# Performance work log

Measured on AMD Instinct MI355X. Metric: run time of the kernel, lower is better.

## Reference

```python
import jax, jax.numpy as jnp
import numpy as np

B, S, H = 2, 2048, 2048
NH, HD = 16, 128


def _rope_tables(seq_len, dim, base=10000.0):
    inv_freq = 1.0 / (base ** (np.arange(0, dim, 2, dtype=np.float32) / dim))
    t = np.arange(seq_len, dtype=np.float32)
    freqs = np.outer(t, inv_freq)                      # [S, dim/2]
    emb = np.concatenate([freqs, freqs], axis=-1)      # [S, dim] (HF convention)
    return jnp.asarray(np.cos(emb)), jnp.asarray(np.sin(emb))


def setup_inputs() -> dict:
    key = jax.random.key(0)
    k1, k2, k3, k4, k5 = jax.random.split(key, 5)
    hidden_states = jax.random.normal(k1, (B, S, H), dtype=jnp.float32)
    # additive causal mask, broadcast over heads: (B, 1, S, S)
    causal = jnp.tril(jnp.ones((S, S), dtype=bool))
    attention_mask = jnp.where(causal, 0.0, -1e9).astype(jnp.float32)
    attention_mask = jnp.broadcast_to(attention_mask[None, None], (B, 1, S, S))
    rope_cos, rope_sin = _rope_tables(S, HD)
    scale = 1.0 / np.sqrt(H)
    Wq = jax.random.normal(k2, (H, H), dtype=jnp.float32) * scale
    Wk = jax.random.normal(k3, (H, H), dtype=jnp.float32) * scale
    Wv = jax.random.normal(k4, (H, H), dtype=jnp.float32) * scale
    Wo = jax.random.normal(k5, (H, H), dtype=jnp.float32) * scale
    return dict(hidden_states=hidden_states, attention_mask=attention_mask,
                rope_cos=rope_cos, rope_sin=rope_sin, Wq=Wq, Wk=Wk, Wv=Wv, Wo=Wo)


def _rotate_half(x):
    half = x.shape[-1] // 2
    return jnp.concatenate([-x[..., half:], x[..., :half]], axis=-1)


def reference(hidden_states, attention_mask, rope_cos, rope_sin, Wq, Wk, Wv, Wo):
    bsz, q_len, _ = hidden_states.shape
    scaling = HD ** -0.5
    # projections (torch Linear: y = x @ W.T)
    q = (hidden_states @ Wq.T).reshape(bsz, q_len, NH, HD).transpose(0, 2, 1, 3)
    k = (hidden_states @ Wk.T).reshape(bsz, q_len, NH, HD).transpose(0, 2, 1, 3)
    v = (hidden_states @ Wv.T).reshape(bsz, q_len, NH, HD).transpose(0, 2, 1, 3)
    # RoPE (rotate_half convention)
    cos = rope_cos[None, None]  # [1,1,S,HD]
    sin = rope_sin[None, None]
    q = q * cos + _rotate_half(q) * sin
    k = k * cos + _rotate_half(k) * sin
    # attention
    scores = jnp.einsum('bhqd,bhkd->bhqk', q, k) * scaling + attention_mask
    attn = jax.nn.softmax(scores.astype(jnp.float32), axis=-1).astype(q.dtype)
    out = jnp.einsum('bhqk,bhkd->bhqd', attn, v)
    out = out.transpose(0, 2, 1, 3).reshape(bsz, q_len, NH * HD)
    return out @ Wo.T
```

## Files before the change

### kernel.cpp

```cpp
#include <hip/hip_runtime.h>
#include <hip/hip_bf16.h>

typedef __bf16 bf16;
typedef __attribute__((ext_vector_type(8))) __bf16 bf16x8;
typedef __attribute__((ext_vector_type(4))) __bf16 bf16x4;
typedef __attribute__((ext_vector_type(4))) float f32x4;

#define BB 2
#define SS 2048
#define HH 2048
#define NH 16
#define HD 128

#define GLOAD_LDS16(g, l)                                                  \
    __builtin_amdgcn_global_load_lds(                                      \
        (const __attribute__((address_space(1))) void*)(g),                \
        (__attribute__((address_space(3))) void*)(l), 16, 0, 0)

__global__ __launch_bounds__(256) void cast_all(const float* __restrict__ hs,
                                                const float* __restrict__ Wq,
                                                const float* __restrict__ Wk,
                                                const float* __restrict__ Wv,
                                                const float* __restrict__ Wo,
                                                bf16* __restrict__ Xb,
                                                bf16* __restrict__ Wqkv,
                                                bf16* __restrict__ Wob) {
    const int XE4 = (BB * SS * HH) / 4;
    const int WE4 = (HH * HH) / 4;
    int i = blockIdx.x * 256 + threadIdx.x;
    const float* src;
    bf16* dst;
    int off;
    if (i < XE4) { src = hs; dst = Xb; off = i; }
    else if (i < XE4 + WE4) { src = Wq; dst = Wqkv; off = i - XE4; }
    else if (i < XE4 + 2 * WE4) { src = Wk; dst = Wqkv + (size_t)HH * HH; off = i - XE4 - WE4; }
    else if (i < XE4 + 3 * WE4) { src = Wv; dst = Wqkv + 2 * (size_t)HH * HH; off = i - XE4 - 2 * WE4; }
    else { src = Wo; dst = Wob; off = i - XE4 - 3 * WE4; }
    f32x4 v = *reinterpret_cast<const f32x4*>(src + (size_t)off * 4);
    bf16x4 o;
    o[0] = (bf16)v[0]; o[1] = (bf16)v[1]; o[2] = (bf16)v[2]; o[3] = (bf16)v[3];
    *reinterpret_cast<bf16x4*>(dst + (size_t)off * 4) = o;
}

__global__ __launch_bounds__(512, 2) void gemm256_qkv(const bf16* __restrict__ A,
                                                      const bf16* __restrict__ B,
                                                      bf16* __restrict__ Cb,
                                                      int M, int N, int K) {
    __shared__ bf16 LA[2][256 * 64];
    __shared__ bf16 LB[2][256 * 64];
    const int tid = threadIdx.x, lane = tid & 63, wave = tid >> 6;
    const int l15 = lane & 15, lhi = lane >> 4;
    const int wr = wave >> 2, wc = wave & 3;
    const int NBY = M >> 8;
    const int cpx = gridDim.x >> 3;
    const int wg = (blockIdx.x & 7) * cpx + (blockIdx.x >> 3);
    const int m0 = (wg % NBY) * 256, n0 = (wg / NBY) * 256;
    const int NK = K >> 6;
    const int xorR = (l15 & 7) << 4;

    auto stageA = [&](int buf, int t, int h) {
        const int k0 = t << 6;
#pragma unroll
        for (int j = 0; j < 2; ++j) {
            int Xw = ((j * 128 + h * 64) << 7) + (wave << 10);
            int X = Xw + lane * 16;
            int T = X ^ (((X >> 7) & 7) << 4);
            GLOAD_LDS16(&A[(size_t)(m0 + (T >> 7)) * K + k0 + ((T & 127) >> 1)],
                        (char*)LA[buf] + Xw);
        }
    };
    auto stageB = [&](int buf, int t, int h) {
        const int k0 = t << 6;
#pragma unroll
        for (int j = 0; j < 2; ++j) {
            int base_row = h * 32 + (2 * j + (wave >> 2)) * 64;
            int Xw = (base_row << 7) + ((wave & 3) << 10);
            int X = Xw + lane * 16;
            int T = X ^ (((X >> 7) & 7) << 4);
            GLOAD_LDS16(&B[(size_t)(n0 + (T >> 7)) * K + k0 + ((T & 127) >> 1)],
                        (char*)LB[buf] + Xw);
        }
    };

    f32x4 acc[8][4] = {};

    stageA(0, 0, 0); stageB(0, 0, 0); stageB(0, 0, 1); stageA(0, 0, 1);
    stageA(1, 1, 0); stageB(1, 1, 1);
    asm volatile("s_waitcnt vmcnt(4)" ::: "memory");
    __builtin_amdgcn_s_barrier();

    bf16x8 af[4][2], bv0[2][2], bv1[2][2];

#pragma unroll 1
    for (int t = 0; t < NK; ++t) {
        const int buf = t & 1;
        char* lA = (char*)LA[buf];
        char* lB = (char*)LB[buf];

#pragma unroll
        for (int f = 0; f < 4; ++f)
#pragma unroll
            for (int ks = 0; ks < 2; ++ks) {
                int T = ((wr * 128 + f * 16 + l15) << 7) + ks * 64 + lhi * 16;
                af[f][ks] = *reinterpret_cast<const bf16x8*>(lA + (T ^ xorR));
            }
#pragma unroll
        for (int g = 0; g < 2; ++g)
#pragma unroll
            for (int ks = 0; ks < 2; ++ks) {
                int T = ((wc * 64 + g * 16 + l15) << 7) + ks * 64 + lhi * 16;
                bv0[g][ks] = *reinterpret_cast<const bf16x8*>(lB + (T ^ xorR));
            }
        if (t + 1 < NK) stageB(buf ^ 1, t + 1, 0);
        __builtin_amdgcn_s_barrier();
        __builtin_amdgcn_s_setprio(1);
#pragma unroll
        for (int f = 0; f < 4; ++f)
#pragma unroll
            for (int g = 0; g < 2; ++g)
#pragma unroll
                for (int ks = 0; ks < 2; ++ks)
                    acc[f][g] = __builtin_amdgcn_mfma_f32_16x16x32_bf16(af[f][ks], bv0[g][ks], acc[f][g], 0, 0, 0);
        __builtin_amdgcn_s_setprio(0);
        __builtin_amdgcn_s_barrier();

#pragma unroll
        for (int g = 0; g < 2; ++g)
#pragma unroll
            for (int ks = 0; ks < 2; ++ks) {
                int T = ((wc * 64 + 32 + g * 16 + l15) << 7) + ks * 64 + lhi * 16;
                bv1[g][ks] = *reinterpret_cast<const bf16x8*>(lB + (T ^ xorR));
            }
        if (t + 1 < NK) stageA(buf ^ 1, t + 1, 1);
        __builtin_amdgcn_s_barrier();
        __builtin_amdgcn_s_setprio(1);
#pragma unroll
        for (int f = 0; f < 4; ++f)
#pragma unroll
            for (int g = 0; g < 2; ++g)
#pragma unroll
                for (int ks = 0; ks < 2; ++ks)
                    acc[f][2 + g] = __builtin_amdgcn_mfma_f32_16x16x32_bf16(af[f][ks], bv1[g][ks], acc[f][2 + g], 0, 0, 0);
        __builtin_amdgcn_s_setprio(0);
        __builtin_amdgcn_s_barrier();

#pragma unroll
        for (int f = 0; f < 4; ++f)
#pragma unroll
            for (int ks = 0; ks < 2; ++ks) {
                int T = ((wr * 128 + 64 + f * 16 + l15) << 7) + ks * 64 + lhi * 16;
                af[f][ks] = *reinterpret_cast<const bf16x8*>(lA + (T ^ xorR));
            }
        if (t + 2 < NK) stageA(buf, t + 2, 0);
        __builtin_amdgcn_s_barrier();
        __builtin_amdgcn_s_setprio(1);
#pragma unroll
        for (int f = 0; f < 4; ++f)
#pragma unroll
            for (int g = 0; g < 2; ++g)
#pragma unroll
                for (int ks = 0; ks < 2; ++ks)
                    acc[4 + f][2 + g] = __builtin_amdgcn_mfma_f32_16x16x32_bf16(af[f][ks], bv1[g][ks], acc[4 + f][2 + g], 0, 0, 0);
        __builtin_amdgcn_s_setprio(0);
        __builtin_amdgcn_s_barrier();

        if (t + 2 < NK) stageB(buf, t + 2, 1);
        __builtin_amdgcn_s_barrier();
        __builtin_amdgcn_s_setprio(1);
#pragma unroll
        for (int f = 0; f < 4; ++f)
#pragma unroll
            for (int g = 0; g < 2; ++g)
#pragma unroll
                for (int ks = 0; ks < 2; ++ks)
                    acc[4 + f][g] = __builtin_amdgcn_mfma_f32_16x16x32_bf16(af[f][ks], bv0[g][ks], acc[4 + f][g], 0, 0, 0);
        __builtin_amdgcn_s_setprio(0);
        if (t + 2 == NK) {
            asm volatile("s_waitcnt vmcnt(0)" ::: "memory");
        } else if (t + 1 < NK) {
            asm volatile("s_waitcnt vmcnt(4)" ::: "memory");
        }
        __builtin_amdgcn_s_barrier();
    }

#pragma unroll
    for (int mf = 0; mf < 8; ++mf)
#pragma unroll
        for (int nf = 0; nf < 4; ++nf)
#pragma unroll
            for (int r = 0; r < 4; ++r) {
                int gm = m0 + wr * 128 + mf * 16 + lhi * 4 + r;
                int gn = n0 + wc * 64 + nf * 16 + l15;
                int proj = gn >> 11, n2 = gn & 2047;
                int b = gm >> 11, s = gm & (SS - 1);
                int h = n2 >> 7, d = n2 & (HD - 1);
                Cb[((size_t)proj << 23) + ((((size_t)(b * NH + h)) * SS + s) << 7) + d] =
                    (bf16)acc[mf][nf][r];
            }
}

__global__ __launch_bounds__(256) void gemm_bt(const bf16* __restrict__ A,
                                               const bf16* __restrict__ B,
                                               float* __restrict__ Cf,
                                               int M, int N, int K) {
    __shared__ bf16 As[128 * 64];
    __shared__ bf16 Bs[128 * 64];
    const int tid = threadIdx.x;
    const int lane = tid & 63, wave = tid >> 6;
    const int l15 = lane & 15, lhi = lane >> 4;
    const int m0 = blockIdx.y * 128, n0 = blockIdx.x * 128;
    const int wm = (wave >> 1) * 64, wn = (wave & 1) * 64;
    const int lrow = lane >> 3;
    const int lcol = (lane & 7) * 8;

    f32x4 acc[4][4] = {};

    for (int k0 = 0; k0 < K; k0 += 64) {
#pragma unroll
        for (int j = 0; j < 4; ++j) {
            const int c = wave * 4 + j;
            const int row = c * 8 + lrow;
            GLOAD_LDS16(&A[(size_t)(m0 + row) * K + k0 + lcol], &As[c * 512]);
            GLOAD_LDS16(&B[(size_t)(n0 + row) * K + k0 + lcol], &Bs[c * 512]);
        }
        __syncthreads();
#pragma unroll
        for (int ks = 0; ks < 2; ++ks) {
            bf16x8 af[4], bfr[4];
#pragma unroll
            for (int i = 0; i < 4; ++i)
                af[i] = *reinterpret_cast<const bf16x8*>(&As[(wm + i * 16 + l15) * 64 + ks * 32 + 8 * lhi]);
#pragma unroll
            for (int j = 0; j < 4; ++j)
                bfr[j] = *reinterpret_cast<const bf16x8*>(&Bs[(wn + j * 16 + l15) * 64 + ks * 32 + 8 * lhi]);
#pragma unroll
            for (int i = 0; i < 4; ++i)
#pragma unroll
                for (int j = 0; j < 4; ++j)
                    acc[i][j] = __builtin_amdgcn_mfma_f32_16x16x32_bf16(af[i], bfr[j], acc[i][j], 0, 0, 0);
        }
        __syncthreads();
    }

#pragma unroll
    for (int i = 0; i < 4; ++i)
#pragma unroll
        for (int j = 0; j < 4; ++j)
#pragma unroll
            for (int r = 0; r < 4; ++r) {
                int gm = m0 + wm + i * 16 + lhi * 4 + r;
                int gn = n0 + wn + j * 16 + l15;
                Cf[(size_t)gm * N + gn] = acc[i][j][r];
            }
}

__global__ __launch_bounds__(256) void rope_tv(bf16* __restrict__ Qh,
                                               bf16* __restrict__ Kh,
                                               const float* __restrict__ cosT,
                                               const float* __restrict__ sinT,
                                               const bf16* __restrict__ Vh,
                                               bf16* __restrict__ Vt) {
    __shared__ bf16 T[64 * 64];
    const int tid = threadIdx.x;
    if (blockIdx.x < 2048) {
        int idx = blockIdx.x * 256 + tid;
        int g = idx & 7;
        int s = (idx >> 3) & (SS - 1);
        int head = idx >> 14;
        int d0 = g * 8;
        size_t base = ((size_t)head * SS + s) * HD;
        f32x4 ca = *reinterpret_cast<const f32x4*>(&cosT[s * HD + d0]);
        f32x4 cb = *reinterpret_cast<const f32x4*>(&cosT[s * HD + d0 + 4]);
        f32x4 sa = *reinterpret_cast<const f32x4*>(&sinT[s * HD + d0]);
        f32x4 sb = *reinterpret_cast<const f32x4*>(&sinT[s * HD + d0 + 4]);
        bf16x8 ql = *reinterpret_cast<const bf16x8*>(&Qh[base + d0]);
        bf16x8 qh = *reinterpret_cast<const bf16x8*>(&Qh[base + 64 + d0]);
        bf16x8 kl = *reinterpret_cast<const bf16x8*>(&Kh[base + d0]);
        bf16x8 kh = *reinterpret_cast<const bf16x8*>(&Kh[base + 64 + d0]);
        bf16x8 qlo, qhi, klo, khi;
#pragma unroll
        for (int j = 0; j < 8; ++j) {
            float c = (j < 4) ? ca[j] : cb[j - 4];
            float sn = (j < 4) ? sa[j] : sb[j - 4];
            float q0 = (float)ql[j], q1 = (float)qh[j];
            float k0 = (float)kl[j], k1 = (float)kh[j];
            qlo[j] = (bf16)(q0 * c - q1 * sn);
            qhi[j] = (bf16)(q1 * c + q0 * sn);
            klo[j] = (bf16)(k0 * c - k1 * sn);
            khi[j] = (bf16)(k1 * c + k0 * sn);
        }
        *reinterpret_cast<bf16x8*>(&Qh[base + d0]) = qlo;
        *reinterpret_cast<bf16x8*>(&Qh[base + 64 + d0]) = qhi;
        *reinterpret_cast<bf16x8*>(&Kh[base + d0]) = klo;
        *reinterpret_cast<bf16x8*>(&Kh[base + 64 + d0]) = khi;
    } else {
        const int b2 = blockIdx.x - 2048;
        const int s0 = (b2 & 31) * 64;
        const int d0 = ((b2 >> 5) & 1) * 64;
        const int head = b2 >> 6;
        const bf16* src = Vh + ((size_t)head * SS) * HD;
        bf16* dst = Vt + ((size_t)head * HD) * SS;

#pragma unroll
        for (int i = 0; i < 2; ++i) {
            int id = tid + i * 256;
            int r = id >> 3, c16 = id & 7;
            bf16x8 v = *reinterpret_cast<const bf16x8*>(&src[(size_t)(s0 + r) * HD + d0 + c16 * 8]);
            int sw = c16 ^ ((r ^ (r >> 3)) & 7);
            *reinterpret_cast<bf16x8*>((char*)T + r * 128 + sw * 16) = v;
        }
        __syncthreads();
#pragma unroll
        for (int i = 0; i < 2; ++i) {
            int id = tid + i * 256;
            int dr = id >> 3, sc8 = (id & 7) * 8;
            bf16x8 o;
#pragma unroll
            for (int j = 0; j < 8; ++j) {
                int r = sc8 + j;
                int sw = (dr >> 3) ^ ((r ^ (r >> 3)) & 7);
                o[j] = *reinterpret_cast<const bf16*>((char*)T + r * 128 + sw * 16 + (dr & 7) * 2);
            }
            *reinterpret_cast<bf16x8*>(&dst[(size_t)(d0 + dr) * SS + s0 + sc8]) = o;
        }
    }
}

__global__ __launch_bounds__(256) void attn_kernel(const bf16* __restrict__ Q,
                                                   const bf16* __restrict__ K,
                                                   const bf16* __restrict__ Vt,
                                                   bf16* __restrict__ Ob) {
    __shared__ bf16 Ks[2][64 * 128];
    __shared__ bf16 Vs[2][128 * 64];
    __shared__ bf16 Ps[4][16][72];

    const int tid = threadIdx.x, lane = tid & 63, wave = tid >> 6;
    const int l15 = lane & 15, lhi = lane >> 4;
    const int bid = blockIdx.x;
    const int orig = (bid & 7) * 64 + (bid >> 3);
    const int head = orig >> 4;
    const int pi = orig & 15;
    const int b = head >> 4, h = head & (NH - 1);
    const size_t hb = (size_t)head * SS * HD;
    const bf16* Vth = Vt + (size_t)head * HD * SS;
    const float cexp = 0.08838834764831845f * 1.4426950408889634f;
    const float THR = 62.0f;

#pragma unroll 1
    for (int part = 0; part < 2; ++part) {
        const int t = part ? (31 - pi) : pi;
        const int q0 = t * 64;
        const int qw = q0 + wave * 16;
        const int nkv = t + 1;

        bf16x8 qf[4];
#pragma unroll
        for (int ks = 0; ks < 4; ++ks)
            qf[ks] = *reinterpret_cast<const bf16x8*>(
                &Q[hb + (size_t)(qw + l15) * HD + ks * 32 + 8 * lhi]);

        f32x4 oacc[8] = {};
        float Mr[4], Lp[4];
#pragma unroll
        for (int r = 0; r < 4; ++r) { Mr[r] = -INFINITY; Lp[r] = 0.f; }

        bf16x8 kr[4], vr[4];
#pragma unroll
        for (int i = 0; i < 4; ++i) {
            int id = tid + i * 256;
            kr[i] = *reinterpret_cast<const bf16x8*>(&K[hb + (size_t)(id >> 4) * HD + (id & 15) * 8]);
            vr[i] = *reinterpret_cast<const bf16x8*>(&Vth[(size_t)(id >> 3) * SS + (id & 7) * 8]);
        }
#pragma unroll
        for (int i = 0; i < 4; ++i) {
            int id = tid + i * 256;
            int krow = id >> 4, kc = id & 15;
            *reinterpret_cast<bf16x8*>((char*)Ks[0] + ((krow * 256 + kc * 16) ^ ((krow & 7) << 4))) = kr[i];
            int vrow = id >> 3, vc = id & 7;
            *reinterpret_cast<bf16x8*>((char*)Vs[0] + ((vrow * 128 + vc * 16) ^ ((vrow & 7) << 4))) = vr[i];
        }
        __syncthreads();

        for (int it = 0; it < nkv; ++it) {
            const int cur = it & 1;
            const bool pre = (it + 1 < nkv);
            if (pre) {
                const int kv0 = (it + 1) * 64;
#pragma unroll
                for (int i = 0; i < 4; ++i) {
                    int id = tid + i * 256;
                    kr[i] = *reinterpret_cast<const bf16x8*>(&K[hb + (size_t)(kv0 + (id >> 4)) * HD + (id & 15) * 8]);
                    vr[i] = *reinterpret_cast<const bf16x8*>(&Vth[(size_t)(id >> 3) * SS + kv0 + (id & 7) * 8]);
                }
            }

            f32x4 sf[4] = {};
#pragma unroll
            for (int ks = 0; ks < 4; ++ks) {
#pragma unroll
                for (int ne = 0; ne < 4; ++ne) {
                    int row = ne * 16 + l15;
                    bf16x8 kf = *reinterpret_cast<const bf16x8*>(
                        (const char*)Ks[cur] + ((row * 256 + (ks * 4 + lhi) * 16) ^ ((row & 7) << 4)));
                    sf[ne] = __builtin_amdgcn_mfma_f32_16x16x32_bf16(qf[ks], kf, sf[ne], 0, 0, 0);
                }
            }

            if (it == nkv - 1) {
#pragma unroll
                for (int ne = 0; ne < 4; ++ne)
#pragma unroll
                    for (int r = 0; r < 4; ++r) {
                        int gq = qw + lhi * 4 + r;
                        int gk = it * 64 + ne * 16 + l15;
                        if (gk > gq) sf[ne][r] = -INFINITY;
                    }
            }

            float lm[4];
#pragma unroll
            for (int r = 0; r < 4; ++r)
                lm[r] = fmaxf(fmaxf(sf[0][r], sf[1][r]), fmaxf(sf[2][r], sf[3][r]));
            bool need = (lm[0] > Mr[0] + THR) || (lm[1] > Mr[1] + THR) ||
                        (lm[2] > Mr[2] + THR) || (lm[3] > Mr[3] + THR);
            if (__any(need)) {
                float rmax[4] = {lm[0], lm[1], lm[2], lm[3]};
#pragma unroll
                for (int m = 1; m < 16; m <<= 1)
#pragma unroll
                    for (int r = 0; r < 4; ++r)
                        rmax[r] = fmaxf(rmax[r], __shfl_xor(rmax[r], m));
#pragma unroll
                for (int r = 0; r < 4; ++r) {
                    float nM = fmaxf(Mr[r], rmax[r]);
                    float scf = __builtin_amdgcn_exp2f((Mr[r] - nM) * cexp);
                    Mr[r] = nM;
                    Lp[r] *= scf;
#pragma unroll
                    for (int nf = 0; nf < 8; ++nf) oacc[nf][r] *= scf;
                }
            }
#pragma unroll
            for (int ne = 0; ne < 4; ++ne)
#pragma unroll
                for (int r = 0; r < 4; ++r) {
                    float p = __builtin_amdgcn_exp2f((sf[ne][r] - Mr[r]) * cexp);
                    Lp[r] += p;
                    Ps[wave][lhi * 4 + r][ne * 16 + l15] = (bf16)p;
                }

#pragma unroll
            for (int ks = 0; ks < 2; ++ks) {
                bf16x8 pa = *reinterpret_cast<const bf16x8*>(&Ps[wave][l15][ks * 32 + 8 * lhi]);
#pragma unroll
                for (int nf = 0; nf < 8; ++nf) {
                    int row = nf * 16 + l15;
                    bf16x8 vb = *reinterpret_cast<const bf16x8*>(
                        (const char*)Vs[cur] + ((row * 128 + (ks * 4 + lhi) * 16) ^ ((row & 7) << 4)));
                    oacc[nf] = __builtin_amdgcn_mfma_f32_16x16x32_bf16(pa, vb, oacc[nf], 0, 0, 0);
                }
            }

            if (pre) {
#pragma unroll
                for (int i = 0; i < 4; ++i) {
                    int id = tid + i * 256;
                    int krow = id >> 4, kc = id & 15;
                    *reinterpret_cast<bf16x8*>((char*)Ks[cur ^ 1] + ((krow * 256 + kc * 16) ^ ((krow & 7) << 4))) = kr[i];
                    int vrow = id >> 3, vc = id & 7;
                    *reinterpret_cast<bf16x8*>((char*)Vs[cur ^ 1] + ((vrow * 128 + vc * 16) ^ ((vrow & 7) << 4))) = vr[i];
                }
            }
            __syncthreads();
        }

#pragma unroll
        for (int m = 1; m < 16; m <<= 1)
#pragma unroll
            for (int r = 0; r < 4; ++r)
                Lp[r] += __shfl_xor(Lp[r], m);
        float inv[4];
#pragma unroll
        for (int r = 0; r < 4; ++r) inv[r] = 1.f / Lp[r];
#pragma unroll
        for (int nf = 0; nf < 8; ++nf)
#pragma unroll
            for (int r = 0; r < 4; ++r) {
                int s = qw + lhi * 4 + r;
                int d = nf * 16 + l15;
                Ob[((size_t)(b * SS + s)) * HH + h * HD + d] = (bf16)(oacc[nf][r] * inv[r]);
            }
    }
}

extern "C" void kernel_launch(void* const* d_in, const int* in_sizes, int n_in,
                              void* d_out, int out_size, void* d_ws, size_t ws_size,
                              hipStream_t stream) {
    const float* hs   = (const float*)d_in[0];
    const float* cosT = (const float*)d_in[2];
    const float* sinT = (const float*)d_in[3];
    const float* Wq   = (const float*)d_in[4];
    const float* Wk   = (const float*)d_in[5];
    const float* Wv   = (const float*)d_in[6];
    const float* Wo   = (const float*)d_in[7];
    float* out = (float*)d_out;

    char* w = (char*)d_ws;
    auto alloc = [&](size_t bytes) {
        char* p = w;
        w += (bytes + 255) & ~(size_t)255;
        return p;
    };
    const size_t XE = (size_t)BB * SS * HH;
    const size_t WE = (size_t)HH * HH;
    bf16* Xb   = (bf16*)alloc(XE * 2);
    bf16* Wqkv = (bf16*)alloc(3 * WE * 2);
    bf16* Wob  = (bf16*)alloc(WE * 2);
    bf16* QKV  = (bf16*)alloc(3 * XE * 2);
    bf16* Vtg  = (bf16*)alloc(XE * 2);
    bf16* Ob   = (bf16*)alloc(XE * 2);

    const int M = BB * SS;
    bf16* Qh = QKV;
    bf16* Kh = QKV + XE;
    bf16* Vh = QKV + 2 * XE;

    {
        int total4 = (int)((XE + 4 * WE) / 4);
        cast_all<<<(total4 + 255) / 256, 256, 0, stream>>>(hs, Wq, Wk, Wv, Wo, Xb, Wqkv, Wob);
    }

    gemm256_qkv<<<dim3((M / 256) * (3 * HH / 256)), 512, 0, stream>>>(Xb, Wqkv, QKV, M, 3 * HH, HH);

    rope_tv<<<4096, 256, 0, stream>>>(Qh, Kh, cosT, sinT, Vh, Vtg);

    attn_kernel<<<512, 256, 0, stream>>>(Qh, Kh, Vtg, Ob);

    dim3 ogrid(HH / 128, M / 128);
    gemm_bt<<<ogrid, 256, 0, stream>>>(Ob, Wob, out, M, HH, HH);
}
```

Before: 298.4 us.

## Use 128-row query tiles with 8 waves and direct global-to-LDS KV staging

Measured after the change: 273.8 us. 1.09x faster.

```diff
diff --git a/kernel.cpp b/kernel.cpp
--- a/kernel.cpp
+++ b/kernel.cpp
@@ -326,32 +326,51 @@
     }
 }
 
-__global__ __launch_bounds__(256) void attn_kernel(const bf16* __restrict__ Q,
+__global__ __launch_bounds__(512) void attn_kernel(const bf16* __restrict__ Q,
                                                    const bf16* __restrict__ K,
                                                    const bf16* __restrict__ Vt,
                                                    bf16* __restrict__ Ob) {
     __shared__ bf16 Ks[2][64 * 128];
     __shared__ bf16 Vs[2][128 * 64];
-    __shared__ bf16 Ps[4][16][72];
+    __shared__ bf16 Ps[8][16 * 72];
 
     const int tid = threadIdx.x, lane = tid & 63, wave = tid >> 6;
     const int l15 = lane & 15, lhi = lane >> 4;
     const int bid = blockIdx.x;
-    const int orig = (bid & 7) * 64 + (bid >> 3);
-    const int head = orig >> 4;
-    const int pi = orig & 15;
+    const int orig = (bid & 7) * 32 + (bid >> 3);
+    const int head = orig >> 3;
+    const int pi = orig & 7;
     const int b = head >> 4, h = head & (NH - 1);
     const size_t hb = (size_t)head * SS * HD;
     const bf16* Vth = Vt + (size_t)head * HD * SS;
     const float cexp = 0.08838834764831845f * 1.4426950408889634f;
     const float THR = 62.0f;
 
+    auto stageKV = [&](int buf, int kv0) {
+#pragma unroll
+        for (int j = 0; j < 2; ++j) {
+            int Xw = (j * 8 + wave) << 10;
+            int X = Xw + lane * 16;
+            int T = X ^ (((X >> 8) & 7) << 4);
+            GLOAD_LDS16(&K[hb + (size_t)(kv0 + (T >> 8)) * HD + ((T & 255) >> 1)],
+                        (char*)Ks[buf] + Xw);
+        }
+#pragma unroll
+        for (int j = 0; j < 2; ++j) {
+            int Xw = (j * 8 + wave) << 10;
+            int X = Xw + lane * 16;
+            int T = X ^ (((X >> 7) & 7) << 4);
+            GLOAD_LDS16(&Vth[(size_t)(T >> 7) * SS + kv0 + ((T & 127) >> 1)],
+                        (char*)Vs[buf] + Xw);
+        }
+    };
+
 #pragma unroll 1
     for (int part = 0; part < 2; ++part) {
-        const int t = part ? (31 - pi) : pi;
-        const int q0 = t * 64;
+        const int t = part ? (15 - pi) : pi;
+        const int q0 = t * 128;
         const int qw = q0 + wave * 16;
-        const int nkv = t + 1;
+        const int nkv = 2 * t + 2;
 
         bf16x8 qf[4];
 #pragma unroll
@@ -364,35 +383,13 @@
 #pragma unroll
         for (int r = 0; r < 4; ++r) { Mr[r] = -INFINITY; Lp[r] = 0.f; }
 
-        bf16x8 kr[4], vr[4];
-#pragma unroll
-        for (int i = 0; i < 4; ++i) {
-            int id = tid + i * 256;
-            kr[i] = *reinterpret_cast<const bf16x8*>(&K[hb + (size_t)(id >> 4) * HD + (id & 15) * 8]);
-            vr[i] = *reinterpret_cast<const bf16x8*>(&Vth[(size_t)(id >> 3) * SS + (id & 7) * 8]);
-        }
-#pragma unroll
-        for (int i = 0; i < 4; ++i) {
-            int id = tid + i * 256;
-            int krow = id >> 4, kc = id & 15;
-            *reinterpret_cast<bf16x8*>((char*)Ks[0] + ((krow * 256 + kc * 16) ^ ((krow & 7) << 4))) = kr[i];
-            int vrow = id >> 3, vc = id & 7;
-            *reinterpret_cast<bf16x8*>((char*)Vs[0] + ((vrow * 128 + vc * 16) ^ ((vrow & 7) << 4))) = vr[i];
-        }
-        __syncthreads();
+        stageKV(0, 0);
+        asm volatile("s_waitcnt vmcnt(0)" ::: "memory");
+        __builtin_amdgcn_s_barrier();
 
         for (int it = 0; it < nkv; ++it) {
             const int cur = it & 1;
-            const bool pre = (it + 1 < nkv);
-            if (pre) {
-                const int kv0 = (it + 1) * 64;
-#pragma unroll
-                for (int i = 0; i < 4; ++i) {
-                    int id = tid + i * 256;
-                    kr[i] = *reinterpret_cast<const bf16x8*>(&K[hb + (size_t)(kv0 + (id >> 4)) * HD + (id & 15) * 8]);
-                    vr[i] = *reinterpret_cast<const bf16x8*>(&Vth[(size_t)(id >> 3) * SS + kv0 + (id & 7) * 8]);
-                }
-            }
+            if (it + 1 < nkv) stageKV(cur ^ 1, (it + 1) * 64);
 
             f32x4 sf[4] = {};
 #pragma unroll
@@ -406,7 +403,7 @@
                 }
             }
 
-            if (it == nkv - 1) {
+            if (it >= nkv - 2) {
 #pragma unroll
                 for (int ne = 0; ne < 4; ++ne)
 #pragma unroll
@@ -446,12 +443,13 @@
                 for (int r = 0; r < 4; ++r) {
                     float p = __builtin_amdgcn_exp2f((sf[ne][r] - Mr[r]) * cexp);
                     Lp[r] += p;
-                    Ps[wave][lhi * 4 + r][ne * 16 + l15] = (bf16)p;
+                    Ps[wave][(lhi * 4 + r) * 72 + ne * 16 + l15] = (bf16)p;
                 }
 
 #pragma unroll
             for (int ks = 0; ks < 2; ++ks) {
-                bf16x8 pa = *reinterpret_cast<const bf16x8*>(&Ps[wave][l15][ks * 32 + 8 * lhi]);
+                bf16x8 pa = *reinterpret_cast<const bf16x8*>(
+                    &Ps[wave][l15 * 72 + ks * 32 + 8 * lhi]);
 #pragma unroll
                 for (int nf = 0; nf < 8; ++nf) {
                     int row = nf * 16 + l15;
@@ -461,17 +459,8 @@
                 }
             }
 
-            if (pre) {
-#pragma unroll
-                for (int i = 0; i < 4; ++i) {
-                    int id = tid + i * 256;
-                    int krow = id >> 4, kc = id & 15;
-                    *reinterpret_cast<bf16x8*>((char*)Ks[cur ^ 1] + ((krow * 256 + kc * 16) ^ ((krow & 7) << 4))) = kr[i];
-                    int vrow = id >> 3, vc = id & 7;
-                    *reinterpret_cast<bf16x8*>((char*)Vs[cur ^ 1] + ((vrow * 128 + vc * 16) ^ ((vrow & 7) << 4))) = vr[i];
-                }
-            }
-            __syncthreads();
+            asm volatile("s_waitcnt vmcnt(0)" ::: "memory");
+            __builtin_amdgcn_s_barrier();
         }
 
 #pragma unroll
@@ -534,7 +523,7 @@
 
     rope_tv<<<4096, 256, 0, stream>>>(Qh, Kh, cosT, sinT, Vh, Vtg);
 
-    attn_kernel<<<512, 256, 0, stream>>>(Qh, Kh, Vtg, Ob);
+    attn_kernel<<<256, 512, 0, stream>>>(Qh, Kh, Vtg, Ob);
 
     dim3 ogrid(HH / 128, M / 128);
     gemm_bt<<<ogrid, 256, 0, stream>>>(Ob, Wob, out, M, HH, HH);
```
